# Kernel optimization log

Hardware: AMD Instinct MI355X
Metric: run time of the kernel (lower is better)

The kernel has to match this reference:

```python
import jax, jax.numpy as jnp
import numpy as np

B, S, D = 8, 4096, 128


def setup_inputs() -> dict:
    key = jax.random.key(0)
    kx, kw = jax.random.split(key)
    x = jax.random.normal(kx, (B, S, D), dtype=jnp.float32)
    W = jax.random.normal(kw, (D, D), dtype=jnp.float32) * 0.05  # 'random_normal' init
    b = jnp.zeros((D,), dtype=jnp.float32)  # created in build() but unused in call()
    return {"x": x, "W": W, "b": b}


def reference(x, W, b):
    # q = a = x @ W  (both projections use the same weight in the source)
    q = jnp.einsum("bsd,de->bse", x, W)
    # scores = q @ a^T -> [B, S, S]; no 1/sqrt(d) scaling in the source
    scores = jnp.einsum("bsd,btd->bst", q, q)
    attn = jax.nn.softmax(scores, axis=-1)
    # output = attn @ inputs (values are the raw inputs, not a projection)
    out = jnp.einsum("bst,btd->bsd", attn, x)
    return out
```

## Files before the change

### kernel.cpp

```cpp
#include <hip/hip_runtime.h>

typedef unsigned short u16;
typedef unsigned int u32;
typedef short s16x8 __attribute__((ext_vector_type(8)));
typedef float f32x4 __attribute__((ext_vector_type(4)));
typedef float f32x16 __attribute__((ext_vector_type(16)));

#define B_  8
#define S_  4096
#define D_  128
#define SOFF 40.0f

#define VOFF  9216
#define BUFSZ 19456
#define SBUF  (2 * BUFSZ)
#define LDSZ  (4 * SBUF)

__device__ __forceinline__ u16 f2bf(float f) {
  union { float f; unsigned u; } v; v.f = f;
  unsigned r = v.u + 0x7fffu + ((v.u >> 16) & 1u);
  return (u16)(r >> 16);
}

__device__ __forceinline__ u32 pack_bf(float a, float b) {
  union { float f; u32 u; } ua, ub;
  ua.f = a; ub.f = b;
  return ((ua.u + 0x8000u) & 0xffff0000u) | ((ub.u + 0x8000u) >> 16);
}

__device__ __forceinline__ void async_cp16(const void* g, void* l) {
  __builtin_amdgcn_global_load_lds(
      (const __attribute__((address_space(1))) void*)g,
      (__attribute__((address_space(3))) void*)l, 16, 0, 0);
}

__global__ __launch_bounds__(256) void prep_kernel(
    const float* __restrict__ x, const float* __restrict__ W,
    u16* __restrict__ qb, u16* __restrict__ vT)
{
  __shared__ u16 xb[32][136];
  __shared__ u16 qs[32][136];
  const int tid  = threadIdx.x;
  const int b    = blockIdx.x & 7;
  const int m0   = (blockIdx.x >> 3) * 32;
  const int lane = tid & 63, wave = tid >> 6;
  const int l32  = lane & 31, hi = lane >> 5;

  const float* xg = x + ((size_t)b * S_ + m0) * D_;
#pragma unroll
  for (int i = 0; i < 4; ++i) {
    int idx = (i * 256 + tid) * 4;
    f32x4 v = *(const f32x4*)(xg + idx);
    int row = idx >> 7, col = idx & 127;
    *(u32*)(&xb[row][col])     = (u32)f2bf(v.x) | ((u32)f2bf(v.y) << 16);
    *(u32*)(&xb[row][col + 2]) = (u32)f2bf(v.z) | ((u32)f2bf(v.w) << 16);
  }
  __syncthreads();

  u16* vTb = vT + (size_t)b * D_ * S_;
#pragma unroll
  for (int i = 0; i < 8; ++i) {
    int oi = i * 256 + tid;
    int d = oi >> 4, jj = oi & 15, t = 2 * jj;
    u32 v = (u32)xb[t][d] | ((u32)xb[t + 1][d] << 16);
    int jjs = (jj & 9) | ((jj & 2) << 1) | ((jj & 4) >> 1);
    ((u32*)(vTb + (size_t)d * S_ + m0))[jjs] = v;
  }

  s16x8 a[8];
#pragma unroll
  for (int f = 0; f < 8; ++f)
    a[f] = *(const s16x8*)(&xb[l32][f * 16 + hi * 8]);
  const int n = wave * 32 + l32;
  f32x16 acc = (f32x16)(0.f);
#pragma unroll
  for (int f = 0; f < 8; ++f) {
    const float* wp = W + (size_t)(f * 16 + hi * 8) * D_ + n;
    float w0 = wp[0 * D_], w1 = wp[1 * D_], w2 = wp[2 * D_], w3 = wp[3 * D_];
    float w4 = wp[4 * D_], w5 = wp[5 * D_], w6 = wp[6 * D_], w7 = wp[7 * D_];
    union { u32 u[4]; s16x8 v; } bfu;
    bfu.u[0] = pack_bf(w1, w0);
    bfu.u[1] = pack_bf(w3, w2);
    bfu.u[2] = pack_bf(w5, w4);
    bfu.u[3] = pack_bf(w7, w6);
    acc = __builtin_amdgcn_mfma_f32_32x32x16_bf16(a[f], bfu.v, acc, 0, 0, 0);
  }
#pragma unroll
  for (int r = 0; r < 16; ++r) {
    int row = (r & 3) + 8 * (r >> 2) + 4 * hi;
    qs[row][wave * 32 + l32] = f2bf(acc[r]);
  }
  __syncthreads();
  u16* qB = qb + ((size_t)b * S_ + m0) * D_;
#pragma unroll
  for (int i = 0; i < 8; ++i) {
    int oi = i * 256 + tid;
    int row = oi >> 6, jj = oi & 63;
    u32 v = (u32)qs[row][2 * jj] | ((u32)qs[row][2 * jj + 1] << 16);
    ((u32*)(qB + (size_t)row * D_))[jj] = v;
  }
}

__global__ __launch_bounds__(512, 2) void flash_kernel(
    const u16* __restrict__ qb, const u16* __restrict__ vT, float* __restrict__ out)
{
  __shared__ __align__(16) char smem[LDSZ];
  const int tid  = threadIdx.x;
  const int wave = tid >> 6, lane = tid & 63;
  const int w4   = wave & 3;
  const int half = wave >> 2;
  const int l32  = lane & 31, hi = lane >> 5;
  const int b    = blockIdx.x & 7;
  const int qt   = blockIdx.x >> 3;

  const u16* qbase = qb + (size_t)b * S_ * D_;
  const u16* vbase = vT + (size_t)b * D_ * S_;
  const u32 hbase = half ? (u32)(2 * SBUF) : 0u;
  const int koff  = half * 2048;

  const char* gp[5]; u32 lp[5]; u32 ksc[5];
#pragma unroll
  for (int sl = 0; sl < 5; ++sl) {
    int j = w4 + 4 * sl;
    if (j < 9) {
      u32 p = (u32)j * 64 + lane; if (p > 543u) p = 543u;
      u32 r = p / 17u; u32 cc = p - r * 17u; if (cc > 15u) cc = 15u;
      gp[sl]  = (const char*)qbase + (size_t)(koff + r) * 256 + cc * 16;
      ksc[sl] = 256; lp[sl] = hbase + (u32)j * 1024;
    } else if (j < 19) {
      u32 i = (u32)j - 9; u32 p = i * 64 + lane;
      u32 r = p / 5u; u32 cc = p - r * 5u; if (cc > 3u) cc = 3u;
      gp[sl]  = (const char*)vbase + (size_t)r * (S_ * 2) + (size_t)koff * 2 + cc * 16;
      ksc[sl] = 2; lp[sl] = hbase + VOFF + i * 1024;
    } else gp[sl] = nullptr;
  }

  s16x8 qf[8];
  {
    const u16* qr = qbase + (size_t)(qt * 128 + w4 * 32 + l32) * D_;
#pragma unroll
    for (int f = 0; f < 8; ++f)
      qf[f] = *(const s16x8*)(qr + f * 16 + hi * 8);
  }

  f32x16 o[4];
#pragma unroll
  for (int dt = 0; dt < 4; ++dt) o[dt] = (f32x16)(0.f);
  float l_i = 0.f;

#pragma unroll
  for (int sl = 0; sl < 5; ++sl)
    if (gp[sl]) async_cp16(gp[sl], smem + lp[sl]);
#pragma unroll
  for (int sl = 0; sl < 5; ++sl)
    if (gp[sl]) async_cp16(gp[sl] + (size_t)32 * ksc[sl], smem + lp[sl] + BUFSZ);
  __syncthreads();

  for (int t = 0; t < 32; ++t) {
    const int sb = t & 1;
    const char* baseA = smem + hbase + (sb ? SBUF : 0u);
    const char* baseB = baseA + BUFSZ;

    s16x8 kfA[8], kfB[8];
#pragma unroll
    for (int f = 0; f < 8; ++f) {
      kfA[f] = *(const s16x8*)(baseA + l32 * 272 + (f * 16 + hi * 8) * 2);
      kfB[f] = *(const s16x8*)(baseB + l32 * 272 + (f * 16 + hi * 8) * 2);
    }

    if (t < 31) {
      u32 k1 = (u32)(2 * t + 2) * 32;
      u32 dst = sb ? 0u : SBUF;
#pragma unroll
      for (int sl = 0; sl < 5; ++sl)
        if (gp[sl]) {
          async_cp16(gp[sl] + (size_t)k1 * ksc[sl], smem + lp[sl] + dst);
          async_cp16(gp[sl] + (size_t)(k1 + 32) * ksc[sl], smem + lp[sl] + dst + BUFSZ);
        }
    }

    f32x16 sA = (f32x16)(-SOFF), sB = (f32x16)(-SOFF);
    __builtin_amdgcn_s_setprio(1);
#pragma unroll
    for (int f = 0; f < 8; ++f) {
      sA = __builtin_amdgcn_mfma_f32_32x32x16_bf16(kfA[f], qf[f], sA, 0, 0, 0);
      sB = __builtin_amdgcn_mfma_f32_32x32x16_bf16(kfB[f], qf[f], sB, 0, 0, 0);
    }
    __builtin_amdgcn_s_setprio(0);

    const char* vbA = baseA + VOFF;
    const char* vbB = baseB + VOFF;
    s16x8 vfA[8], vfB[8];
#pragma unroll
    for (int dt = 0; dt < 4; ++dt)
#pragma unroll
      for (int kh = 0; kh < 2; ++kh) {
        vfA[dt * 2 + kh] = *(const s16x8*)(vbA + (dt * 32 + l32) * 80 + kh * 32 + hi * 16);
        vfB[dt * 2 + kh] = *(const s16x8*)(vbB + (dt * 32 + l32) * 80 + kh * 32 + hi * 16);
      }

    float eA[16], eB[16];
#pragma unroll
    for (int r = 0; r < 16; ++r) { eA[r] = __expf(sA[r]); eB[r] = __expf(sB[r]); }

    float psA = (((eA[0]+eA[1])+(eA[2]+eA[3]))+((eA[4]+eA[5])+(eA[6]+eA[7])))
              + (((eA[8]+eA[9])+(eA[10]+eA[11]))+((eA[12]+eA[13])+(eA[14]+eA[15])));
    float psB = (((eB[0]+eB[1])+(eB[2]+eB[3]))+((eB[4]+eB[5])+(eB[6]+eB[7])))
              + (((eB[8]+eB[9])+(eB[10]+eB[11]))+((eB[12]+eB[13])+(eB[14]+eB[15])));
    float ps = psA + psB;
    ps += __shfl_xor(ps, 32, 64);
    l_i += ps;

    union { u32 u[4]; s16x8 v; } pf0A, pf1A, pf0B, pf1B;
    pf0A.u[0] = pack_bf(eA[1],  eA[0]);
    pf0A.u[1] = pack_bf(eA[3],  eA[2]);
    pf0A.u[2] = pack_bf(eA[5],  eA[4]);
    pf0A.u[3] = pack_bf(eA[7],  eA[6]);
    pf1A.u[0] = pack_bf(eA[9],  eA[8]);
    pf1A.u[1] = pack_bf(eA[11], eA[10]);
    pf1A.u[2] = pack_bf(eA[13], eA[12]);
    pf1A.u[3] = pack_bf(eA[15], eA[14]);
    pf0B.u[0] = pack_bf(eB[1],  eB[0]);
    pf0B.u[1] = pack_bf(eB[3],  eB[2]);
    pf0B.u[2] = pack_bf(eB[5],  eB[4]);
    pf0B.u[3] = pack_bf(eB[7],  eB[6]);
    pf1B.u[0] = pack_bf(eB[9],  eB[8]);
    pf1B.u[1] = pack_bf(eB[11], eB[10]);
    pf1B.u[2] = pack_bf(eB[13], eB[12]);
    pf1B.u[3] = pack_bf(eB[15], eB[14]);

    __builtin_amdgcn_s_setprio(1);
#pragma unroll
    for (int dt = 0; dt < 4; ++dt) {
      o[dt] = __builtin_amdgcn_mfma_f32_32x32x16_bf16(vfA[dt * 2 + 0], pf0A.v, o[dt], 0, 0, 0);
      o[dt] = __builtin_amdgcn_mfma_f32_32x32x16_bf16(vfA[dt * 2 + 1], pf1A.v, o[dt], 0, 0, 0);
      o[dt] = __builtin_amdgcn_mfma_f32_32x32x16_bf16(vfB[dt * 2 + 0], pf0B.v, o[dt], 0, 0, 0);
      o[dt] = __builtin_amdgcn_mfma_f32_32x32x16_bf16(vfB[dt * 2 + 1], pf1B.v, o[dt], 0, 0, 0);
    }
    __builtin_amdgcn_s_setprio(0);

    __syncthreads();
  }

  float (*lo)[132] = (float (*)[132])smem;
  float* ll = (float*)(smem + 128 * 132 * 4);

  if (half == 1) {
#pragma unroll
    for (int dt = 0; dt < 4; ++dt)
#pragma unroll
      for (int r = 0; r < 16; ++r) {
        int d = dt * 32 + (r & 3) + 8 * (r >> 2) + 4 * hi;
        lo[w4 * 32 + l32][d] = o[dt][r];
      }
    if (hi == 0) ll[w4 * 32 + l32] = l_i;
  }
  __syncthreads();
  if (half == 0) {
    float lt  = l_i + ll[w4 * 32 + l32];
    float inv = 1.0f / lt;
#pragma unroll
    for (int dt = 0; dt < 4; ++dt)
#pragma unroll
      for (int r = 0; r < 16; ++r) {
        int d = dt * 32 + (r & 3) + 8 * (r >> 2) + 4 * hi;
        float* p = &lo[w4 * 32 + l32][d];
        *p = (o[dt][r] + *p) * inv;
      }
  }
  __syncthreads();
  {
    float* ob = out + ((size_t)b * S_ + qt * 128) * D_;
#pragma unroll
    for (int i = 0; i < 8; ++i) {
      int flat = (i * 512 + tid) * 4;
      int row = flat >> 7, d = flat & 127;
      *(f32x4*)(ob + flat) = *(const f32x4*)(&lo[row][d]);
    }
  }
}

extern "C" void kernel_launch(void* const* d_in, const int* in_sizes, int n_in,
                              void* d_out, int out_size, void* d_ws, size_t ws_size,
                              hipStream_t stream) {
  const float* x = (const float*)d_in[0];
  const float* W = (const float*)d_in[1];
  float* out = (float*)d_out;

  u16* qb  = (u16*)d_ws;
  u16* vT  = qb + (size_t)B_ * S_ * D_;

  prep_kernel<<<8 * (S_ / 32), 256, 0, stream>>>(x, W, qb, vT);
  flash_kernel<<<8 * (S_ / 128), 512, 0, stream>>>(qb, vT, out);
}
```

Baseline: 159.5 us.

## Specialize waves into QK-softmax producers and PV consumers with LDS P handoff

The flash kernel no longer splits the key range between two wave halves. Waves 0-3 now compute QK^T scores and exponentials, writing bf16 probabilities into a double-buffered LDS slot, while waves 4-7 run the PV MFMAs one iteration behind using a triple-buffered V stage. This removes the final cross-half merge of partial outputs and aims to overlap exp/softmax work with the PV matrix work. The cost is a larger LDS footprint (139 KB, which likely caps occupancy at one block per CU despite launch bounds of 2), extra LDS traffic for P, and a pipeline fill and drain step. The V transpose swizzle in the prep kernel is dropped to match the new layout.

Result: no change. 160.4 us (+0.6%).

```diff
diff --git a/kernel.cpp b/kernel.cpp
--- a/kernel.cpp
+++ b/kernel.cpp
@@ -3,6 +3,7 @@
 typedef unsigned short u16;
 typedef unsigned int u32;
 typedef short s16x8 __attribute__((ext_vector_type(8)));
+typedef unsigned int u32x2 __attribute__((ext_vector_type(2)));
 typedef float f32x4 __attribute__((ext_vector_type(4)));
 typedef float f32x16 __attribute__((ext_vector_type(16)));
 
@@ -11,10 +12,13 @@
 #define D_  128
 #define SOFF 40.0f
 
-#define VOFF  9216
-#define BUFSZ 19456
-#define SBUF  (2 * BUFSZ)
-#define LDSZ  (4 * SBUF)
+#define KSLOT 18432
+#define VBASE 36864
+#define VSLOT 20480
+#define PBASE 98304
+#define PTILE 2560
+#define PSLOT 20480
+#define LDSZ  139264
 
 __device__ __forceinline__ u16 f2bf(float f) {
   union { float f; unsigned u; } v; v.f = f;
@@ -63,8 +67,7 @@
     int oi = i * 256 + tid;
     int d = oi >> 4, jj = oi & 15, t = 2 * jj;
     u32 v = (u32)xb[t][d] | ((u32)xb[t + 1][d] << 16);
-    int jjs = (jj & 9) | ((jj & 2) << 1) | ((jj & 4) >> 1);
-    ((u32*)(vTb + (size_t)d * S_ + m0))[jjs] = v;
+    ((u32*)(vTb + (size_t)d * S_ + m0))[jj] = v;
   }
 
   s16x8 a[8];
@@ -107,37 +110,53 @@
   __shared__ __align__(16) char smem[LDSZ];
   const int tid  = threadIdx.x;
   const int wave = tid >> 6, lane = tid & 63;
-  const int w4   = wave & 3;
-  const int half = wave >> 2;
+  const bool isS = wave < 4;
+  const int q    = wave & 3;
   const int l32  = lane & 31, hi = lane >> 5;
   const int b    = blockIdx.x & 7;
   const int qt   = blockIdx.x >> 3;
 
   const u16* qbase = qb + (size_t)b * S_ * D_;
   const u16* vbase = vT + (size_t)b * D_ * S_;
-  const u32 hbase = half ? (u32)(2 * SBUF) : 0u;
-  const int koff  = half * 2048;
-
-  const char* gp[5]; u32 lp[5]; u32 ksc[5];
+
+  const char* gp[5]; u32 lp[5], ksc[5]; bool isV[5];
 #pragma unroll
   for (int sl = 0; sl < 5; ++sl) {
-    int j = w4 + 4 * sl;
-    if (j < 9) {
-      u32 p = (u32)j * 64 + lane; if (p > 543u) p = 543u;
-      u32 r = p / 17u; u32 cc = p - r * 17u; if (cc > 15u) cc = 15u;
-      gp[sl]  = (const char*)qbase + (size_t)(koff + r) * 256 + cc * 16;
-      ksc[sl] = 256; lp[sl] = hbase + (u32)j * 1024;
-    } else if (j < 19) {
-      u32 i = (u32)j - 9; u32 p = i * 64 + lane;
-      u32 r = p / 5u; u32 cc = p - r * 5u; if (cc > 3u) cc = 3u;
-      gp[sl]  = (const char*)vbase + (size_t)r * (S_ * 2) + (size_t)koff * 2 + cc * 16;
-      ksc[sl] = 2; lp[sl] = hbase + VOFF + i * 1024;
-    } else gp[sl] = nullptr;
-  }
+    int j = wave + 8 * sl;
+    gp[sl] = nullptr;
+    if (j < 38) {
+      int X  = (j >= 19);
+      int jj = j - X * 19;
+      if (jj < 9) {
+        u32 p = (u32)jj * 64 + lane; if (p > 543u) p = 543u;
+        u32 r = p / 17u; u32 cc = p - r * 17u; if (cc > 15u) cc = 15u;
+        gp[sl]  = (const char*)qbase + (size_t)(X * 32 + r) * 256 + cc * 16;
+        ksc[sl] = 16384;
+        lp[sl]  = (u32)X * 9216 + (u32)jj * 1024;
+        isV[sl] = false;
+      } else {
+        u32 i2 = (u32)jj - 9; u32 p = i2 * 64 + lane;
+        u32 r = p / 5u; u32 cc = p - r * 5u; if (cc > 3u) cc = 3u;
+        gp[sl]  = (const char*)vbase + (size_t)r * 8192 + X * 64 + cc * 16;
+        ksc[sl] = 128;
+        lp[sl]  = (u32)X * 10240 + i2 * 1024;
+        isV[sl] = true;
+      }
+    }
+  }
+
+  auto STAGE = [&](int pair) {
+    u32 ks = (u32)(pair & 1) * KSLOT;
+    u32 vs = VBASE + (u32)(pair % 3) * VSLOT;
+#pragma unroll
+    for (int sl = 0; sl < 5; ++sl)
+      if (gp[sl]) async_cp16(gp[sl] + (size_t)pair * ksc[sl],
+                             smem + (isV[sl] ? vs : ks) + lp[sl]);
+  };
 
   s16x8 qf[8];
-  {
-    const u16* qr = qbase + (size_t)(qt * 128 + w4 * 32 + l32) * D_;
+  if (isS) {
+    const u16* qr = qbase + (size_t)(qt * 128 + q * 32 + l32) * D_;
 #pragma unroll
     for (int f = 0; f < 8; ++f)
       qf[f] = *(const s16x8*)(qr + f * 16 + hi * 8);
@@ -148,125 +167,92 @@
   for (int dt = 0; dt < 4; ++dt) o[dt] = (f32x16)(0.f);
   float l_i = 0.f;
 
-#pragma unroll
-  for (int sl = 0; sl < 5; ++sl)
-    if (gp[sl]) async_cp16(gp[sl], smem + lp[sl]);
-#pragma unroll
-  for (int sl = 0; sl < 5; ++sl)
-    if (gp[sl]) async_cp16(gp[sl] + (size_t)32 * ksc[sl], smem + lp[sl] + BUFSZ);
-  __syncthreads();
-
-  for (int t = 0; t < 32; ++t) {
-    const int sb = t & 1;
-    const char* baseA = smem + hbase + (sb ? SBUF : 0u);
-    const char* baseB = baseA + BUFSZ;
-
-    s16x8 kfA[8], kfB[8];
-#pragma unroll
-    for (int f = 0; f < 8; ++f) {
-      kfA[f] = *(const s16x8*)(baseA + l32 * 272 + (f * 16 + hi * 8) * 2);
-      kfB[f] = *(const s16x8*)(baseB + l32 * 272 + (f * 16 + hi * 8) * 2);
-    }
-
-    if (t < 31) {
-      u32 k1 = (u32)(2 * t + 2) * 32;
-      u32 dst = sb ? 0u : SBUF;
-#pragma unroll
-      for (int sl = 0; sl < 5; ++sl)
-        if (gp[sl]) {
-          async_cp16(gp[sl] + (size_t)k1 * ksc[sl], smem + lp[sl] + dst);
-          async_cp16(gp[sl] + (size_t)(k1 + 32) * ksc[sl], smem + lp[sl] + dst + BUFSZ);
-        }
-    }
-
-    f32x16 sA = (f32x16)(-SOFF), sB = (f32x16)(-SOFF);
+  auto STILE = [&](const char* kb, char* pb) {
+    s16x8 kf[8];
+#pragma unroll
+    for (int f = 0; f < 8; ++f)
+      kf[f] = *(const s16x8*)(kb + l32 * 272 + (f * 16 + hi * 8) * 2);
+    f32x16 s = (f32x16)(-SOFF);
     __builtin_amdgcn_s_setprio(1);
 #pragma unroll
-    for (int f = 0; f < 8; ++f) {
-      sA = __builtin_amdgcn_mfma_f32_32x32x16_bf16(kfA[f], qf[f], sA, 0, 0, 0);
-      sB = __builtin_amdgcn_mfma_f32_32x32x16_bf16(kfB[f], qf[f], sB, 0, 0, 0);
-    }
+    for (int f = 0; f < 8; ++f)
+      s = __builtin_amdgcn_mfma_f32_32x32x16_bf16(kf[f], qf[f], s, 0, 0, 0);
     __builtin_amdgcn_s_setprio(0);
-
-    const char* vbA = baseA + VOFF;
-    const char* vbB = baseB + VOFF;
-    s16x8 vfA[8], vfB[8];
-#pragma unroll
-    for (int dt = 0; dt < 4; ++dt)
-#pragma unroll
-      for (int kh = 0; kh < 2; ++kh) {
-        vfA[dt * 2 + kh] = *(const s16x8*)(vbA + (dt * 32 + l32) * 80 + kh * 32 + hi * 16);
-        vfB[dt * 2 + kh] = *(const s16x8*)(vbB + (dt * 32 + l32) * 80 + kh * 32 + hi * 16);
-      }
-
-    float eA[16], eB[16];
-#pragma unroll
-    for (int r = 0; r < 16; ++r) { eA[r] = __expf(sA[r]); eB[r] = __expf(sB[r]); }
-
-    float psA = (((eA[0]+eA[1])+(eA[2]+eA[3]))+((eA[4]+eA[5])+(eA[6]+eA[7])))
-              + (((eA[8]+eA[9])+(eA[10]+eA[11]))+((eA[12]+eA[13])+(eA[14]+eA[15])));
-    float psB = (((eB[0]+eB[1])+(eB[2]+eB[3]))+((eB[4]+eB[5])+(eB[6]+eB[7])))
-              + (((eB[8]+eB[9])+(eB[10]+eB[11]))+((eB[12]+eB[13])+(eB[14]+eB[15])));
-    float ps = psA + psB;
+    float e[16];
+#pragma unroll
+    for (int r = 0; r < 16; ++r) e[r] = __expf(s[r]);
+    float ps = (((e[0] + e[1]) + (e[2] + e[3])) + ((e[4] + e[5]) + (e[6] + e[7])))
+             + (((e[8] + e[9]) + (e[10] + e[11])) + ((e[12] + e[13]) + (e[14] + e[15])));
     ps += __shfl_xor(ps, 32, 64);
     l_i += ps;
-
-    union { u32 u[4]; s16x8 v; } pf0A, pf1A, pf0B, pf1B;
-    pf0A.u[0] = pack_bf(eA[1],  eA[0]);
-    pf0A.u[1] = pack_bf(eA[3],  eA[2]);
-    pf0A.u[2] = pack_bf(eA[5],  eA[4]);
-    pf0A.u[3] = pack_bf(eA[7],  eA[6]);
-    pf1A.u[0] = pack_bf(eA[9],  eA[8]);
-    pf1A.u[1] = pack_bf(eA[11], eA[10]);
-    pf1A.u[2] = pack_bf(eA[13], eA[12]);
-    pf1A.u[3] = pack_bf(eA[15], eA[14]);
-    pf0B.u[0] = pack_bf(eB[1],  eB[0]);
-    pf0B.u[1] = pack_bf(eB[3],  eB[2]);
-    pf0B.u[2] = pack_bf(eB[5],  eB[4]);
-    pf0B.u[3] = pack_bf(eB[7],  eB[6]);
-    pf1B.u[0] = pack_bf(eB[9],  eB[8]);
-    pf1B.u[1] = pack_bf(eB[11], eB[10]);
-    pf1B.u[2] = pack_bf(eB[13], eB[12]);
-    pf1B.u[3] = pack_bf(eB[15], eB[14]);
-
+    char* pw = pb + l32 * 80 + 8 * hi;
+#pragma unroll
+    for (int k = 0; k < 4; ++k) {
+      u32x2 w;
+      w.x = pack_bf(e[4 * k + 1], e[4 * k]);
+      w.y = pack_bf(e[4 * k + 3], e[4 * k + 2]);
+      *(u32x2*)(pw + 16 * k) = w;
+    }
+  };
+
+  auto PVTILE = [&](const char* vb, const char* pb) {
+    s16x8 pf0 = *(const s16x8*)(pb + l32 * 80 + 16 * hi);
+    s16x8 pf1 = *(const s16x8*)(pb + l32 * 80 + 32 + 16 * hi);
+    s16x8 vf[8];
+#pragma unroll
+    for (int dt = 0; dt < 4; ++dt)
+#pragma unroll
+      for (int kh = 0; kh < 2; ++kh)
+        vf[dt * 2 + kh] = *(const s16x8*)(vb + (dt * 32 + l32) * 80 + kh * 32 + hi * 16);
     __builtin_amdgcn_s_setprio(1);
 #pragma unroll
     for (int dt = 0; dt < 4; ++dt) {
-      o[dt] = __builtin_amdgcn_mfma_f32_32x32x16_bf16(vfA[dt * 2 + 0], pf0A.v, o[dt], 0, 0, 0);
-      o[dt] = __builtin_amdgcn_mfma_f32_32x32x16_bf16(vfA[dt * 2 + 1], pf1A.v, o[dt], 0, 0, 0);
-      o[dt] = __builtin_amdgcn_mfma_f32_32x32x16_bf16(vfB[dt * 2 + 0], pf0B.v, o[dt], 0, 0, 0);
-      o[dt] = __builtin_amdgcn_mfma_f32_32x32x16_bf16(vfB[dt * 2 + 1], pf1B.v, o[dt], 0, 0, 0);
+      o[dt] = __builtin_amdgcn_mfma_f32_32x32x16_bf16(vf[dt * 2 + 0], pf0, o[dt], 0, 0, 0);
+      o[dt] = __builtin_amdgcn_mfma_f32_32x32x16_bf16(vf[dt * 2 + 1], pf1, o[dt], 0, 0, 0);
     }
     __builtin_amdgcn_s_setprio(0);
-
+  };
+
+  STAGE(0);
+  __syncthreads();
+
+  for (int i = 0; i < 64; ++i) {
+    if (i < 63) STAGE(i + 1);
+    if (isS) {
+      const char* kb = smem + (u32)(i & 1) * KSLOT;
+      char* pslot = smem + PBASE + (u32)(i & 1) * PSLOT;
+      STILE(kb,        pslot + (u32)q * PTILE);
+      STILE(kb + 9216, pslot + (u32)(4 + q) * PTILE);
+    } else if (i > 0) {
+      const int pj = i - 1;
+      const char* vb = smem + VBASE + (u32)(pj % 3) * VSLOT;
+      const char* pslot = smem + PBASE + (u32)(pj & 1) * PSLOT;
+      PVTILE(vb,         pslot + (u32)q * PTILE);
+      PVTILE(vb + 10240, pslot + (u32)(4 + q) * PTILE);
+    }
     __syncthreads();
   }
+  if (!isS) {
+    const char* vb = smem + VBASE + (u32)(63 % 3) * VSLOT;
+    const char* pslot = smem + PBASE + (u32)(63 & 1) * PSLOT;
+    PVTILE(vb,         pslot + (u32)q * PTILE);
+    PVTILE(vb + 10240, pslot + (u32)(4 + q) * PTILE);
+  }
+  __syncthreads();
 
   float (*lo)[132] = (float (*)[132])smem;
   float* ll = (float*)(smem + 128 * 132 * 4);
 
-  if (half == 1) {
+  if (!isS) {
 #pragma unroll
     for (int dt = 0; dt < 4; ++dt)
 #pragma unroll
       for (int r = 0; r < 16; ++r) {
         int d = dt * 32 + (r & 3) + 8 * (r >> 2) + 4 * hi;
-        lo[w4 * 32 + l32][d] = o[dt][r];
+        lo[q * 32 + l32][d] = o[dt][r];
       }
-    if (hi == 0) ll[w4 * 32 + l32] = l_i;
-  }
-  __syncthreads();
-  if (half == 0) {
-    float lt  = l_i + ll[w4 * 32 + l32];
-    float inv = 1.0f / lt;
-#pragma unroll
-    for (int dt = 0; dt < 4; ++dt)
-#pragma unroll
-      for (int r = 0; r < 16; ++r) {
-        int d = dt * 32 + (r & 3) + 8 * (r >> 2) + 4 * hi;
-        float* p = &lo[w4 * 32 + l32][d];
-        *p = (o[dt][r] + *p) * inv;
-      }
+  } else if (hi == 0) {
+    ll[q * 32 + l32] = l_i;
   }
   __syncthreads();
   {
@@ -275,7 +261,10 @@
     for (int i = 0; i < 8; ++i) {
       int flat = (i * 512 + tid) * 4;
       int row = flat >> 7, d = flat & 127;
-      *(f32x4*)(ob + flat) = *(const f32x4*)(&lo[row][d]);
+      float inv = 1.0f / ll[row];
+      f32x4 v = *(const f32x4*)(&lo[row][d]);
+      v.x *= inv; v.y *= inv; v.z *= inv; v.w *= inv;
+      *(f32x4*)(ob + flat) = v;
     }
   }
 }
```

## Fuse prep and flash kernels with a global atomic grid barrier

Applied to the files above, without the earlier changes.

Merges the projection/transpose prep stage into the flash-attention kernel as a prologue. Each 512-thread block processes its own 128 query rows in two 32-row passes, then spins on a global atomic counter until all 256 blocks finish before starting attention. This removes one kernel launch and the gap between kernels, but it adds a hipMemsetAsync, a grid-wide spin barrier that relies on all 256 blocks being co-resident, and extra syncthreads in the prologue.

After: 184.5 us. 1.16x slower.

```diff
diff --git a/kernel.cpp b/kernel.cpp
--- a/kernel.cpp
+++ b/kernel.cpp
@@ -34,77 +34,10 @@
       (__attribute__((address_space(3))) void*)l, 16, 0, 0);
 }
 
-__global__ __launch_bounds__(256) void prep_kernel(
-    const float* __restrict__ x, const float* __restrict__ W,
-    u16* __restrict__ qb, u16* __restrict__ vT)
+__device__ __forceinline__ void flash_body(
+    const u16* __restrict__ qb, const u16* __restrict__ vT,
+    float* __restrict__ out, char* smem)
 {
-  __shared__ u16 xb[32][136];
-  __shared__ u16 qs[32][136];
-  const int tid  = threadIdx.x;
-  const int b    = blockIdx.x & 7;
-  const int m0   = (blockIdx.x >> 3) * 32;
-  const int lane = tid & 63, wave = tid >> 6;
-  const int l32  = lane & 31, hi = lane >> 5;
-
-  const float* xg = x + ((size_t)b * S_ + m0) * D_;
-#pragma unroll
-  for (int i = 0; i < 4; ++i) {
-    int idx = (i * 256 + tid) * 4;
-    f32x4 v = *(const f32x4*)(xg + idx);
-    int row = idx >> 7, col = idx & 127;
-    *(u32*)(&xb[row][col])     = (u32)f2bf(v.x) | ((u32)f2bf(v.y) << 16);
-    *(u32*)(&xb[row][col + 2]) = (u32)f2bf(v.z) | ((u32)f2bf(v.w) << 16);
-  }
-  __syncthreads();
-
-  u16* vTb = vT + (size_t)b * D_ * S_;
-#pragma unroll
-  for (int i = 0; i < 8; ++i) {
-    int oi = i * 256 + tid;
-    int d = oi >> 4, jj = oi & 15, t = 2 * jj;
-    u32 v = (u32)xb[t][d] | ((u32)xb[t + 1][d] << 16);
-    int jjs = (jj & 9) | ((jj & 2) << 1) | ((jj & 4) >> 1);
-    ((u32*)(vTb + (size_t)d * S_ + m0))[jjs] = v;
-  }
-
-  s16x8 a[8];
-#pragma unroll
-  for (int f = 0; f < 8; ++f)
-    a[f] = *(const s16x8*)(&xb[l32][f * 16 + hi * 8]);
-  const int n = wave * 32 + l32;
-  f32x16 acc = (f32x16)(0.f);
-#pragma unroll
-  for (int f = 0; f < 8; ++f) {
-    const float* wp = W + (size_t)(f * 16 + hi * 8) * D_ + n;
-    float w0 = wp[0 * D_], w1 = wp[1 * D_], w2 = wp[2 * D_], w3 = wp[3 * D_];
-    float w4 = wp[4 * D_], w5 = wp[5 * D_], w6 = wp[6 * D_], w7 = wp[7 * D_];
-    union { u32 u[4]; s16x8 v; } bfu;
-    bfu.u[0] = pack_bf(w1, w0);
-    bfu.u[1] = pack_bf(w3, w2);
-    bfu.u[2] = pack_bf(w5, w4);
-    bfu.u[3] = pack_bf(w7, w6);
-    acc = __builtin_amdgcn_mfma_f32_32x32x16_bf16(a[f], bfu.v, acc, 0, 0, 0);
-  }
-#pragma unroll
-  for (int r = 0; r < 16; ++r) {
-    int row = (r & 3) + 8 * (r >> 2) + 4 * hi;
-    qs[row][wave * 32 + l32] = f2bf(acc[r]);
-  }
-  __syncthreads();
-  u16* qB = qb + ((size_t)b * S_ + m0) * D_;
-#pragma unroll
-  for (int i = 0; i < 8; ++i) {
-    int oi = i * 256 + tid;
-    int row = oi >> 6, jj = oi & 63;
-    u32 v = (u32)qs[row][2 * jj] | ((u32)qs[row][2 * jj + 1] << 16);
-    ((u32*)(qB + (size_t)row * D_))[jj] = v;
-  }
-}
-
-__global__ __launch_bounds__(512, 2) void flash_kernel(
-    const u16* __restrict__ qb, const u16* __restrict__ vT, float* __restrict__ out)
-{
-  __shared__ __align__(16) char smem[LDSZ];
   const int tid  = threadIdx.x;
   const int wave = tid >> 6, lane = tid & 63;
   const int w4   = wave & 3;
@@ -280,6 +213,172 @@
   }
 }
 
+__global__ __launch_bounds__(512, 2) void fused_kernel(
+    const float* __restrict__ x, const float* __restrict__ W,
+    u16* __restrict__ qb, u16* __restrict__ vT,
+    unsigned* __restrict__ ctr, float* __restrict__ out)
+{
+  __shared__ __align__(16) char smem[LDSZ];
+  const int tid  = threadIdx.x;
+  const int b    = blockIdx.x & 7;
+  const int qt   = blockIdx.x >> 3;
+  const int lane = tid & 63;
+  const int l32  = lane & 31, hi = lane >> 5;
+
+  {
+    const int g     = tid >> 8;
+    const int t256  = tid & 255;
+    const int wave4 = (tid >> 6) & 3;
+    u16 (*xb)[136] = (u16 (*)[136])(smem + (size_t)g * 8704);
+    u16 (*qs)[136] = (u16 (*)[136])(smem + 17408 + (size_t)g * 8704);
+    u16* vTb = vT + (size_t)b * D_ * S_;
+
+    for (int p = 0; p < 2; ++p) {
+      const int m0 = qt * 128 + (p * 2 + g) * 32;
+      const float* xg = x + ((size_t)b * S_ + m0) * D_;
+#pragma unroll
+      for (int i = 0; i < 4; ++i) {
+        int idx = (i * 256 + t256) * 4;
+        f32x4 v = *(const f32x4*)(xg + idx);
+        int row = idx >> 7, col = idx & 127;
+        *(u32*)(&xb[row][col])     = (u32)f2bf(v.x) | ((u32)f2bf(v.y) << 16);
+        *(u32*)(&xb[row][col + 2]) = (u32)f2bf(v.z) | ((u32)f2bf(v.w) << 16);
+      }
+      __syncthreads();
+
+#pragma unroll
+      for (int i = 0; i < 8; ++i) {
+        int oi = i * 256 + t256;
+        int d = oi >> 4, jj = oi & 15, t2 = 2 * jj;
+        u32 v = (u32)xb[t2][d] | ((u32)xb[t2 + 1][d] << 16);
+        int jjs = (jj & 9) | ((jj & 2) << 1) | ((jj & 4) >> 1);
+        ((u32*)(vTb + (size_t)d * S_ + m0))[jjs] = v;
+      }
+
+      s16x8 a[8];
+#pragma unroll
+      for (int f = 0; f < 8; ++f)
+        a[f] = *(const s16x8*)(&xb[l32][f * 16 + hi * 8]);
+      const int n = wave4 * 32 + l32;
+      f32x16 acc = (f32x16)(0.f);
+#pragma unroll
+      for (int f = 0; f < 8; ++f) {
+        const float* wp = W + (size_t)(f * 16 + hi * 8) * D_ + n;
+        float w0 = wp[0 * D_], w1 = wp[1 * D_], w2 = wp[2 * D_], w3 = wp[3 * D_];
+        float w4 = wp[4 * D_], w5 = wp[5 * D_], w6 = wp[6 * D_], w7 = wp[7 * D_];
+        union { u32 u[4]; s16x8 v; } bfu;
+        bfu.u[0] = pack_bf(w1, w0);
+        bfu.u[1] = pack_bf(w3, w2);
+        bfu.u[2] = pack_bf(w5, w4);
+        bfu.u[3] = pack_bf(w7, w6);
+        acc = __builtin_amdgcn_mfma_f32_32x32x16_bf16(a[f], bfu.v, acc, 0, 0, 0);
+      }
+#pragma unroll
+      for (int r = 0; r < 16; ++r) {
+        int row = (r & 3) + 8 * (r >> 2) + 4 * hi;
+        qs[row][wave4 * 32 + l32] = f2bf(acc[r]);
+      }
+      __syncthreads();
+
+      u16* qB = qb + ((size_t)b * S_ + m0) * D_;
+#pragma unroll
+      for (int i = 0; i < 8; ++i) {
+        int oi = i * 256 + t256;
+        int row = oi >> 6, jj = oi & 63;
+        u32 v = (u32)qs[row][2 * jj] | ((u32)qs[row][2 * jj + 1] << 16);
+        ((u32*)(qB + (size_t)row * D_))[jj] = v;
+      }
+      __syncthreads();
+    }
+  }
+
+  if (tid == 0) {
+    __hip_atomic_fetch_add(ctr, 1u, __ATOMIC_RELEASE, __HIP_MEMORY_SCOPE_AGENT);
+    for (long it = 0; it < (1L << 26); ++it) {
+      if (__hip_atomic_load(ctr, __ATOMIC_ACQUIRE, __HIP_MEMORY_SCOPE_AGENT) >= 256u)
+        break;
+      __builtin_amdgcn_s_sleep(32);
+    }
+  }
+  __syncthreads();
+
+  flash_body(qb, vT, out, smem);
+}
+
+__global__ __launch_bounds__(256) void prep_kernel(
+    const float* __restrict__ x, const float* __restrict__ W,
+    u16* __restrict__ qb, u16* __restrict__ vT)
+{
+  __shared__ u16 xb[32][136];
+  __shared__ u16 qs[32][136];
+  const int tid  = threadIdx.x;
+  const int b    = blockIdx.x & 7;
+  const int m0   = (blockIdx.x >> 3) * 32;
+  const int lane = tid & 63, wave = tid >> 6;
+  const int l32  = lane & 31, hi = lane >> 5;
+
+  const float* xg = x + ((size_t)b * S_ + m0) * D_;
+#pragma unroll
+  for (int i = 0; i < 4; ++i) {
+    int idx = (i * 256 + tid) * 4;
+    f32x4 v = *(const f32x4*)(xg + idx);
+    int row = idx >> 7, col = idx & 127;
+    *(u32*)(&xb[row][col])     = (u32)f2bf(v.x) | ((u32)f2bf(v.y) << 16);
+    *(u32*)(&xb[row][col + 2]) = (u32)f2bf(v.z) | ((u32)f2bf(v.w) << 16);
+  }
+  __syncthreads();
+
+  u16* vTb = vT + (size_t)b * D_ * S_;
+#pragma unroll
+  for (int i = 0; i < 8; ++i) {
+    int oi = i * 256 + tid;
+    int d = oi >> 4, jj = oi & 15, t = 2 * jj;
+    u32 v = (u32)xb[t][d] | ((u32)xb[t + 1][d] << 16);
+    int jjs = (jj & 9) | ((jj & 2) << 1) | ((jj & 4) >> 1);
+    ((u32*)(vTb + (size_t)d * S_ + m0))[jjs] = v;
+  }
+
+  s16x8 a[8];
+#pragma unroll
+  for (int f = 0; f < 8; ++f)
+    a[f] = *(const s16x8*)(&xb[l32][f * 16 + hi * 8]);
+  const int n = wave * 32 + l32;
+  f32x16 acc = (f32x16)(0.f);
+#pragma unroll
+  for (int f = 0; f < 8; ++f) {
+    const float* wp = W + (size_t)(f * 16 + hi * 8) * D_ + n;
+    float w0 = wp[0 * D_], w1 = wp[1 * D_], w2 = wp[2 * D_], w3 = wp[3 * D_];
+    float w4 = wp[4 * D_], w5 = wp[5 * D_], w6 = wp[6 * D_], w7 = wp[7 * D_];
+    union { u32 u[4]; s16x8 v; } bfu;
+    bfu.u[0] = pack_bf(w1, w0);
+    bfu.u[1] = pack_bf(w3, w2);
+    bfu.u[2] = pack_bf(w5, w4);
+    bfu.u[3] = pack_bf(w7, w6);
+    acc = __builtin_amdgcn_mfma_f32_32x32x16_bf16(a[f], bfu.v, acc, 0, 0, 0);
+  }
+#pragma unroll
+  for (int r = 0; r < 16; ++r) {
+    int row = (r & 3) + 8 * (r >> 2) + 4 * hi;
+    qs[row][wave * 32 + l32] = f2bf(acc[r]);
+  }
+  __syncthreads();
+  u16* qB = qb + ((size_t)b * S_ + m0) * D_;
+#pragma unroll
+  for (int i = 0; i < 8; ++i) {
+    int oi = i * 256 + tid;
+    int row = oi >> 6, jj = oi & 63;
+    u32 v = (u32)qs[row][2 * jj] | ((u32)qs[row][2 * jj + 1] << 16);
+    ((u32*)(qB + (size_t)row * D_))[jj] = v;
+  }
+}
+
+__global__ __launch_bounds__(512, 2) void flash_kernel(
+    const u16* __restrict__ qb, const u16* __restrict__ vT, float* __restrict__ out)
+{
+  __shared__ __align__(16) char smem[LDSZ];
+  flash_body(qb, vT, out, smem);
+}
+
 extern "C" void kernel_launch(void* const* d_in, const int* in_sizes, int n_in,
                               void* d_out, int out_size, void* d_ws, size_t ws_size,
                               hipStream_t stream) {
@@ -289,7 +388,14 @@
 
   u16* qb  = (u16*)d_ws;
   u16* vT  = qb + (size_t)B_ * S_ * D_;
-
-  prep_kernel<<<8 * (S_ / 32), 256, 0, stream>>>(x, W, qb, vT);
-  flash_kernel<<<8 * (S_ / 128), 512, 0, stream>>>(qb, vT, out);
-}
+  const size_t base = 2 * (size_t)B_ * S_ * D_ * sizeof(u16);
+  unsigned* ctr = (unsigned*)((char*)d_ws + base);
+
+  if (ws_size >= base + 64) {
+    hipMemsetAsync(ctr, 0, sizeof(unsigned), stream);
+    fused_kernel<<<8 * (S_ / 128), 512, 0, stream>>>(x, W, qb, vT, ctr, out);
+  } else {
+    prep_kernel<<<8 * (S_ / 32), 256, 0, stream>>>(x, W, qb, vT);
+    flash_kernel<<<8 * (S_ / 128), 512, 0, stream>>>(qb, vT, out);
+  }
+}
```
